# Optimization experiments

Hardware: AMD Instinct MI355X
Metric: run time of the kernel (lower is better)

The kernel has to match this reference:

```python
import jax, jax.numpy as jnp
import numpy as np

H = 128; L = 3; ODIM = 400; SCALE = 30.0

def gather_nodes(h, E_idx):
    # h: [B,N,C], E_idx: [B,N,K] -> [B,N,K,C]
    B, N, K = E_idx.shape
    C = h.shape[-1]
    idx = jnp.broadcast_to(E_idx.reshape(B, N * K, 1), (B, N * K, C))
    return jnp.take_along_axis(h, idx, axis=1).reshape(B, N, K, C)

def layer_norm(x, eps=1e-5):
    mu = jnp.mean(x, axis=-1, keepdims=True)
    var = jnp.mean((x - mu) ** 2, axis=-1, keepdims=True)
    return (x - mu) / jnp.sqrt(var + eps)

def merge_dups(h_E, inv_mapping):
    # h_E: [B,N,K,C]; inv_mapping: [B,N*K]
    B, N, K, C = h_E.shape
    flat = h_E.reshape(B, N * K, C)
    idx = jnp.broadcast_to(inv_mapping[:, :, None], (B, N * K, C))
    return jnp.take_along_axis(flat, idx, axis=1).reshape(B, N, K, C)

def setup_inputs() -> dict:
    key = jax.random.key(0)
    ks = jax.random.split(key, 40)
    B, N, K = 2, 1024, 30
    d = {}
    d['h_V0'] = jax.random.normal(ks[0], (B, N, H), jnp.float32)
    d['h_E0'] = jax.random.normal(ks[1], (B, N, K, H), jnp.float32)
    d['E_idx'] = jax.random.randint(ks[2], (B, N, K), 0, N, jnp.int32)
    d['inv_mapping'] = jax.random.randint(ks[3], (B, N * K), 0, N * K, jnp.int32)
    d['x_mask'] = jnp.ones((B, N), jnp.float32)
    s = 0.05
    d['Wv_w'] = jax.random.normal(ks[4], (H, H)) * s; d['Wv_b'] = jnp.zeros((H,))
    d['We_w'] = jax.random.normal(ks[5], (H, H)) * s; d['We_b'] = jnp.zeros((H,))
    # node MPNN layers: message MLP (3h->h->h->h) + dense FFN (h->4h->h), stacked [L,...]
    d['nW1'] = jax.random.normal(ks[6], (L, 3 * H, H)) * s; d['nb1'] = jnp.zeros((L, H))
    d['nW2'] = jax.random.normal(ks[7], (L, H, H)) * s;     d['nb2'] = jnp.zeros((L, H))
    d['nW3'] = jax.random.normal(ks[8], (L, H, H)) * s;     d['nb3'] = jnp.zeros((L, H))
    d['nWd1'] = jax.random.normal(ks[9], (L, H, 4 * H)) * s; d['nbd1'] = jnp.zeros((L, 4 * H))
    d['nWd2'] = jax.random.normal(ks[10], (L, 4 * H, H)) * s; d['nbd2'] = jnp.zeros((L, H))
    # edge MPNN layers
    d['eW1'] = jax.random.normal(ks[11], (L, 3 * H, H)) * s; d['eb1'] = jnp.zeros((L, H))
    d['eW2'] = jax.random.normal(ks[12], (L, H, H)) * s;     d['eb2'] = jnp.zeros((L, H))
    d['eW3'] = jax.random.normal(ks[13], (L, H, H)) * s;     d['eb3'] = jnp.zeros((L, H))
    d['eWd1'] = jax.random.normal(ks[14], (L, H, 4 * H)) * s; d['ebd1'] = jnp.zeros((L, 4 * H))
    d['eWd2'] = jax.random.normal(ks[15], (L, 4 * H, H)) * s; d['ebd2'] = jnp.zeros((L, H))
    d['Wout_w'] = jax.random.normal(ks[16], (H, ODIM)) * s; d['Wout_b'] = jnp.zeros((ODIM,))
    return d

def reference(h_V0, h_E0, E_idx, inv_mapping, x_mask,
              Wv_w, Wv_b, We_w, We_b,
              nW1, nb1, nW2, nb2, nW3, nb3, nWd1, nbd1, nWd2, nbd2,
              eW1, eb1, eW2, eb2, eW3, eb3, eWd1, ebd1, eWd2, ebd2,
              Wout_w, Wout_b):
    B, N, K = E_idx.shape
    h_V = h_V0 @ Wv_w + Wv_b                      # W_v embedding
    h_E = h_E0 @ We_w + We_b                      # W_e embedding
    mask_attend = gather_nodes(x_mask[..., None], E_idx)[..., 0] * x_mask[..., None]  # [B,N,K]
    for l in range(L):
        # ---- node update (NodeMPNNLayer) ----
        h_nb = gather_nodes(h_V, E_idx)                           # [B,N,K,H]
        h_i = jnp.broadcast_to(h_V[:, :, None, :], h_nb.shape)
        h_EV = jnp.concatenate([h_i, h_nb, h_E], axis=-1)         # [B,N,K,3H]
        m = jax.nn.relu(h_EV @ nW1[l] + nb1[l])
        m = jax.nn.relu(m @ nW2[l] + nb2[l])
        m = m @ nW3[l] + nb3[l]
        m = m * mask_attend[..., None]
        dh = jnp.sum(m, axis=-2) / SCALE
        h_V = layer_norm(h_V + dh)
        dh = jax.nn.relu(h_V @ nWd1[l] + nbd1[l]) @ nWd2[l] + nbd2[l]
        h_V = layer_norm(h_V + dh)
        h_V = h_V * x_mask[..., None]
        # ---- edge update (EdgeMPNNLayer) ----
        h_j = gather_nodes(h_V, E_idx)
        h_i = jnp.broadcast_to(h_V[:, :, None, :], h_j.shape)
        h_EV = jnp.concatenate([h_i, h_E, h_j], axis=-1)          # [B,N,K,3H]
        m = jax.nn.relu(h_EV @ eW1[l] + eb1[l])
        m = jax.nn.relu(m @ eW2[l] + eb2[l])
        m = m @ eW3[l] + eb3[l]
        h_E = layer_norm(h_E + m)
        dh = jax.nn.relu(h_E @ eWd1[l] + ebd1[l]) @ eWd2[l] + ebd2[l]
        h_E = layer_norm(h_E + dh)
        h_E = h_E * mask_attend[..., None]
    etab = h_E @ Wout_w + Wout_b                                  # [B,N,K,400]
    etab = merge_dups(etab, inv_mapping)
    return etab
```

## Files before the change

### kernel.cpp

```cpp
#include <hip/hip_runtime.h>
#include <hip/hip_bf16.h>
#include <stdint.h>


typedef __bf16 bf16_t;
typedef __attribute__((ext_vector_type(8))) __bf16 bf16x8;
typedef __attribute__((ext_vector_type(4))) float f32x4;

#define B_    2
#define N_    1024
#define KN    30
#define H_    128
#define L_    3
#define ODIM_ 400
#define NK    (N_ * KN)
#define RT    (B_ * N_ * KN)
#define BN_   (B_ * N_)

#define EPI_PLAIN 0
#define EPI_RELU  1
#define EPI_F32   2
#define EPI_LN    4
#define EPI_OUT   5

__device__ __forceinline__ float wred(float v) {
#pragma unroll
  for (int off = 32; off > 0; off >>= 1) v += __shfl_xor(v, off, 64);
  return v;
}

__device__ __forceinline__ void gld16(const bf16_t* g, bf16_t* l) {
  __builtin_amdgcn_global_load_lds(
      (__attribute__((address_space(1))) void*)(g),
      (__attribute__((address_space(3))) void*)(l), 16, 0, 0);
}

template<int NI>
__device__ __forceinline__ void mmN(const bf16_t* __restrict__ Ah,
                                    const bf16_t* __restrict__ Bh,
                                    int wm, int wn, int fm, int q, int fx,
                                    f32x4 (&acc)[4][NI])
{
#pragma unroll
  for (int h = 0; h < 2; ++h) {
    const int slot = ((((h << 2) | q) ^ fx) << 3);
    bf16x8 af[4], bfv[NI];
#pragma unroll
    for (int mi = 0; mi < 4; ++mi)
      af[mi] = *reinterpret_cast<const bf16x8*>(
          &Ah[(wm * 64 + mi * 16 + fm) * 64 + slot]);
#pragma unroll
    for (int ni = 0; ni < NI; ++ni)
      bfv[ni] = *reinterpret_cast<const bf16x8*>(
          &Bh[(wn * (NI * 16) + ni * 16 + fm) * 64 + slot]);
#pragma unroll
    for (int mi = 0; mi < 4; ++mi)
#pragma unroll
      for (int ni = 0; ni < NI; ++ni)
        acc[mi][ni] = __builtin_amdgcn_mfma_f32_16x16x32_bf16(
            af[mi], bfv[ni], acc[mi][ni], 0, 0, 0);
  }
}

struct GCArgs {
  const bf16_t* Ain;
  const bf16_t* W1; int koff1; int ldw1;
  const bf16_t* W2; const bf16_t* b2;
  const bf16_t* W3; const bf16_t* b3;
  const float* U; const float* G; const int* E;
  const float* ma;
  float* Agg;
  const bf16_t* Wd1; const bf16_t* bd1;
  const bf16_t* Wd2; const bf16_t* bd2;
  const float* mvec;
  bf16_t* outF;
  const bf16_t* Wug; const bf16_t* bug;
  float* Uo; float* Go;
};

template<int MODE>
__global__ __launch_bounds__(256, 2) void gc(GCArgs a)
{
  __shared__ __align__(16) bf16_t bufA[2][8192];
  __shared__ __align__(16) bf16_t bufB[2][8192];
  __shared__ __align__(16) bf16_t Ws[8192];
  float* lnS  = (float*)Ws;
  float* lnS2 = lnS + 256;
  float* aggS = (float*)Ws;

  const int tid = threadIdx.x;
  const int w = tid >> 6, l = tid & 63;
  const int wm = w & 1, wn = w >> 1;
  const int row0 = blockIdx.x * 128;
  const int lr = l >> 3;
  const int kg8 = ((l & 7) ^ lr) << 3;
  const int fm = l & 15, q = l >> 4, fx = fm & 7;

  auto stage128 = [&](const bf16_t* W, int ldw, int koff) {
    const bf16_t* gb = W + (size_t)(w * 32 + lr) * ldw + koff + kg8;
#pragma unroll
    for (int s = 0; s < 4; ++s)
      gld16(gb + (size_t)(s * 8) * ldw, &Ws[w * 2048 + s * 512]);
  };
  auto stage64 = [&](const bf16_t* W, int ldw, int koff) {
    const bf16_t* gb = W + (size_t)(w * 16 + lr) * ldw + koff + kg8;
#pragma unroll
    for (int s = 0; s < 2; ++s)
      gld16(gb + (size_t)(s * 8) * ldw, &Ws[w * 1024 + s * 512]);
  };

  auto do_gemm = [&](const bf16_t* SRC, const bf16_t* W, int koff, int ldw,
                     f32x4 (&acc)[4][4]) {
#pragma unroll
    for (int kt = 0; kt < 2; ++kt) {
      __syncthreads();
      stage128(W, ldw, koff + kt * 64);
      __syncthreads();
      mmN<4>(SRC + kt * 8192, Ws, wm, wn, fm, q, fx, acc);
    }
  };

  auto wb = [&](f32x4 (&acc)[4][4], bf16_t* dst) {
#pragma unroll
    for (int mi = 0; mi < 4; ++mi)
#pragma unroll
      for (int rr = 0; rr < 4; ++rr) {
        int row = wm * 64 + mi * 16 + q * 4 + rr;
#pragma unroll
        for (int ni = 0; ni < 4; ++ni) {
          int cl = ni * 16 + fm;
          dst[wn * 8192 + row * 64 +
              ((((cl >> 3) ^ (row & 7)) << 3) | (cl & 7))] =
              (bf16_t)acc[mi][ni][rr];
        }
      }
  };

  {
    bf16_t* dst = (MODE == 2) ? bufB[0] : bufA[0];
    const bf16_t* gb = a.Ain + (size_t)(row0 + w * 32 + lr) * 128 + kg8;
#pragma unroll
    for (int kt = 0; kt < 2; ++kt)
#pragma unroll
      for (int s = 0; s < 4; ++s)
        gld16(gb + (size_t)(s * 8) * 128 + kt * 64,
              dst + kt * 8192 + w * 2048 + s * 512);
  }

  if constexpr (MODE <= 1) {
    f32x4 acc1[4][4] = {};
    do_gemm(bufA[0], a.W1, a.koff1, a.ldw1, acc1);
#pragma unroll
    for (int mi = 0; mi < 4; ++mi)
#pragma unroll
      for (int rr = 0; rr < 4; ++rr) {
        int rg = row0 + wm * 64 + mi * 16 + q * 4 + rr;
        const float* Ur = a.U + (size_t)(rg / KN) * 128;
        const float* Gr = a.G + (size_t)((rg / NK) * N_ + a.E[rg]) * 128;
#pragma unroll
        for (int ni = 0; ni < 4; ++ni) {
          int col = wn * 64 + ni * 16 + fm;
          acc1[mi][ni][rr] = fmaxf(acc1[mi][ni][rr] + Ur[col] + Gr[col], 0.f);
        }
      }
    wb(acc1, bufB[0]);

    f32x4 acc2[4][4] = {};
    do_gemm(bufB[0], a.W2, 0, 128, acc2);
#pragma unroll
    for (int mi = 0; mi < 4; ++mi)
#pragma unroll
      for (int rr = 0; rr < 4; ++rr)
#pragma unroll
        for (int ni = 0; ni < 4; ++ni) {
          int col = wn * 64 + ni * 16 + fm;
          acc2[mi][ni][rr] = fmaxf(acc2[mi][ni][rr] + (float)a.b2[col], 0.f);
        }
    __syncthreads();
    wb(acc2, bufB[0]);

    f32x4 acc3[4][4] = {};
    do_gemm(bufB[0], a.W3, 0, 128, acc3);

    if constexpr (MODE == 0) {
      __syncthreads();
      for (int i = tid; i < 768; i += 256) aggS[i] = 0.f;
      __syncthreads();
      const int nb0 = row0 / KN;
#pragma unroll
      for (int mi = 0; mi < 4; ++mi)
#pragma unroll
        for (int rr = 0; rr < 4; ++rr) {
          int rg = row0 + wm * 64 + mi * 16 + q * 4 + rr;
          float mav = a.ma[rg];
          int nl = rg / KN - nb0;
#pragma unroll
          for (int ni = 0; ni < 4; ++ni) {
            int col = wn * 64 + ni * 16 + fm;
            atomicAdd(&aggS[nl * 128 + col],
                      (acc3[mi][ni][rr] + (float)a.b3[col]) * mav);
          }
        }
      __syncthreads();
      const int nbL = (row0 + 127) / KN;
      for (int i = tid; i < 768; i += 256) {
        int ng = nb0 + (i >> 7);
        if (ng <= nbL)
          atomicAdd(&a.Agg[(size_t)ng * 128 + (i & 127)], aggS[i]);
      }
      return;
    } else {
      __syncthreads();
#pragma unroll
      for (int mi = 0; mi < 4; ++mi)
#pragma unroll
        for (int rr = 0; rr < 4; ++rr) {
          int lrow = wm * 64 + mi * 16 + q * 4 + rr;
          float s = 0.f, s2 = 0.f;
#pragma unroll
          for (int ni = 0; ni < 4; ++ni) {
            int cl = ni * 16 + fm;
            float rv = (float)bufA[wn][lrow * 64 +
                ((((cl >> 3) ^ (lrow & 7)) << 3) | (cl & 7))];
            float v = acc3[mi][ni][rr] + (float)a.b3[wn * 64 + cl] + rv;
            acc3[mi][ni][rr] = v;
            s += v; s2 += v * v;
          }
#pragma unroll
          for (int d = 1; d < 16; d <<= 1) {
            s += __shfl_xor(s, d, 64); s2 += __shfl_xor(s2, d, 64);
          }
          if (fm == (mi * 4 + rr)) { lnS[wn * 128 + lrow] = s;
                                     lnS2[wn * 128 + lrow] = s2; }
        }
      __syncthreads();
#pragma unroll
      for (int mi = 0; mi < 4; ++mi)
#pragma unroll
        for (int rr = 0; rr < 4; ++rr) {
          int lrow = wm * 64 + mi * 16 + q * 4 + rr;
          float st = lnS[lrow] + lnS[128 + lrow];
          float st2 = lnS2[lrow] + lnS2[128 + lrow];
          float mu = st * (1.f / 128.f);
          float var = fmaxf(st2 * (1.f / 128.f) - mu * mu, 0.f);
          float rstd = rsqrtf(var + 1e-5f);
#pragma unroll
          for (int ni = 0; ni < 4; ++ni) {
            int cl = ni * 16 + fm;
            bufB[wn][lrow * 64 +
                ((((cl >> 3) ^ (lrow & 7)) << 3) | (cl & 7))] =
                (bf16_t)((acc3[mi][ni][rr] - mu) * rstd);
          }
        }
    }
  }

  {
    f32x4 accF[4][4] = {};
#pragma unroll 1
    for (int c = 0; c < 8; ++c) {
      const bf16_t* W1c = a.Wd1 + (size_t)(c * 64) * 128;
      f32x4 accH[4][2] = {};
#pragma unroll
      for (int kt = 0; kt < 2; ++kt) {
        __syncthreads();
        stage64(W1c, 128, kt * 64);
        __syncthreads();
        mmN<2>(bufB[0] + kt * 8192, Ws, wm, wn, fm, q, fx, accH);
      }
#pragma unroll
      for (int mi = 0; mi < 4; ++mi)
#pragma unroll
        for (int rr = 0; rr < 4; ++rr) {
          int row = wm * 64 + mi * 16 + q * 4 + rr;
#pragma unroll
          for (int ni = 0; ni < 2; ++ni) {
            int cH = wn * 32 + ni * 16 + fm;
            float hv = fmaxf(accH[mi][ni][rr] +
                             (float)a.bd1[c * 64 + cH], 0.f);
            bufA[0][row * 64 +
                ((((cH >> 3) ^ (row & 7)) << 3) | (cH & 7))] = (bf16_t)hv;
          }
        }
      __syncthreads();
      stage128(a.Wd2, 512, c * 64);
      __syncthreads();
      mmN<4>(bufA[0], Ws, wm, wn, fm, q, fx, accF);
    }

    __syncthreads();
#pragma unroll
    for (int mi = 0; mi < 4; ++mi)
#pragma unroll
      for (int rr = 0; rr < 4; ++rr) {
        int lrow = wm * 64 + mi * 16 + q * 4 + rr;
        float s = 0.f, s2 = 0.f;
#pragma unroll
        for (int ni = 0; ni < 4; ++ni) {
          int cl = ni * 16 + fm;
          float xv = (float)bufB[wn][lrow * 64 +
              ((((cl >> 3) ^ (lrow & 7)) << 3) | (cl & 7))];
          float v = accF[mi][ni][rr] + (float)a.bd2[wn * 64 + cl] + xv;
          accF[mi][ni][rr] = v;
          s += v; s2 += v * v;
        }
#pragma unroll
        for (int d = 1; d < 16; d <<= 1) {
          s += __shfl_xor(s, d, 64); s2 += __shfl_xor(s2, d, 64);
        }
        if (fm == (mi * 4 + rr)) { lnS[wn * 128 + lrow] = s;
                                   lnS2[wn * 128 + lrow] = s2; }
      }
    __syncthreads();
#pragma unroll
    for (int mi = 0; mi < 4; ++mi)
#pragma unroll
      for (int rr = 0; rr < 4; ++rr) {
        int lrow = wm * 64 + mi * 16 + q * 4 + rr;
        size_t rg = (size_t)(row0 + lrow);
        float st = lnS[lrow] + lnS[128 + lrow];
        float st2 = lnS2[lrow] + lnS2[128 + lrow];
        float mu = st * (1.f / 128.f);
        float var = fmaxf(st2 * (1.f / 128.f) - mu * mu, 0.f);
        float rstd = rsqrtf(var + 1e-5f);
        float mk = a.mvec[rg];
#pragma unroll
        for (int ni = 0; ni < 4; ++ni) {
          int col = wn * 64 + ni * 16 + fm;
          float ov = (accF[mi][ni][rr] - mu) * rstd * mk;
          a.outF[rg * 128 + col] = (bf16_t)ov;
          if constexpr (MODE == 2) accF[mi][ni][rr] = ov;
        }
      }

    if constexpr (MODE == 2) {
      __syncthreads();
      wb(accF, bufB[0]);
      f32x4 accU[4][4] = {};
      do_gemm(bufB[0], a.Wug, 0, 384, accU);
#pragma unroll
      for (int mi = 0; mi < 4; ++mi)
#pragma unroll
        for (int rr = 0; rr < 4; ++rr) {
          size_t rg = (size_t)(row0 + wm * 64 + mi * 16 + q * 4 + rr);
#pragma unroll
          for (int ni = 0; ni < 4; ++ni) {
            int col = wn * 64 + ni * 16 + fm;
            a.Uo[rg * 128 + col] = accU[mi][ni][rr] + (float)a.bug[col];
          }
        }
      f32x4 accG[4][4] = {};
      do_gemm(bufB[0], a.Wug, 256, 384, accG);
#pragma unroll
      for (int mi = 0; mi < 4; ++mi)
#pragma unroll
        for (int rr = 0; rr < 4; ++rr) {
          size_t rg = (size_t)(row0 + wm * 64 + mi * 16 + q * 4 + rr);
#pragma unroll
          for (int ni = 0; ni < 4; ++ni) {
            int col = wn * 64 + ni * 16 + fm;
            a.Go[rg * 128 + col] = accG[mi][ni][rr];
          }
        }
    }
  }
}

__global__ __launch_bounds__(256) void gk(
    const bf16_t* __restrict__ A, int lda,
    const bf16_t* __restrict__ Bt, int ldb, int koff,
    const bf16_t* __restrict__ bias,
    int N, int K, int epi,
    bf16_t* __restrict__ C,
    float* __restrict__ Cf, float* __restrict__ Cf1, int koff1,
    const float* __restrict__ U, const float* __restrict__ G,
    const int* __restrict__ E_idx,
    bf16_t* __restrict__ resid, const float* __restrict__ mvec, int row0g,
    const int* __restrict__ inv, const int* __restrict__ flag,
    void* __restrict__ outp)
{
  __shared__ __align__(16) bf16_t As[128 * 64];
  __shared__ __align__(16) bf16_t Bs[128 * 64];
  __shared__ float lnS[2][128];
  __shared__ float lnS2[2][128];

  float* CfD = Cf;
  if (epi == EPI_F32 && blockIdx.z == 1) { koff = koff1; bias = nullptr; CfD = Cf1; }

  const int tid = threadIdx.x;
  const int w = tid >> 6, l = tid & 63;
  const int wm = w & 1, wn = w >> 1;
  const int row0 = blockIdx.y * 128;
  const int col0 = blockIdx.x * 128;
  const int lr = l >> 3;
  const int kg8 = ((l & 7) ^ lr) << 3;

  const bf16_t* ap[4];
  const bf16_t* bp[4];
#pragma unroll
  for (int s = 0; s < 4; ++s) {
    int rA = row0 + w * 32 + s * 8 + lr;
    const bf16_t* abase;
    if (epi == EPI_OUT) {
      int bb = rA / NK;
      abase = A + (size_t)(bb * NK + inv[rA]) * lda;
    } else {
      abase = A + (size_t)rA * lda;
    }
    ap[s] = abase + kg8;
    int rB = col0 + w * 32 + s * 8 + lr;
    if (rB >= N) rB = N - 1;
    bp[s] = Bt + (size_t)rB * ldb + koff + kg8;
  }

  const int fm = l & 15, q = l >> 4, fx = fm & 7;
  f32x4 acc[4][4] = {};

  for (int kt = 0; kt < K; kt += 64) {
    __syncthreads();
#pragma unroll
    for (int s = 0; s < 4; ++s)
      gld16(ap[s] + kt, &As[w * 2048 + s * 512]);
#pragma unroll
    for (int s = 0; s < 4; ++s)
      gld16(bp[s] + kt, &Bs[w * 2048 + s * 512]);
    __syncthreads();
#pragma unroll
    for (int h = 0; h < 2; ++h) {
      bf16x8 af[4], bfv[4];
#pragma unroll
      for (int mi = 0; mi < 4; ++mi)
        af[mi] = *reinterpret_cast<const bf16x8*>(
            &As[(wm * 64 + mi * 16 + fm) * 64 + ((((h << 2) | q) ^ fx) << 3)]);
#pragma unroll
      for (int ni = 0; ni < 4; ++ni)
        bfv[ni] = *reinterpret_cast<const bf16x8*>(
            &Bs[(wn * 64 + ni * 16 + fm) * 64 + ((((h << 2) | q) ^ fx) << 3)]);
#pragma unroll
      for (int mi = 0; mi < 4; ++mi)
#pragma unroll
        for (int ni = 0; ni < 4; ++ni)
          acc[mi][ni] = __builtin_amdgcn_mfma_f32_16x16x32_bf16(
              af[mi], bfv[ni], acc[mi][ni], 0, 0, 0);
    }
  }

  if (epi <= EPI_F32) {
#pragma unroll
    for (int ni = 0; ni < 4; ++ni) {
      int col = col0 + wn * 64 + ni * 16 + fm;
      if (col >= N) continue;
      float bv = bias ? (float)bias[col] : 0.f;
#pragma unroll
      for (int mi = 0; mi < 4; ++mi)
#pragma unroll
        for (int rr = 0; rr < 4; ++rr) {
          size_t rg = (size_t)(row0g + row0 + wm * 64 + mi * 16 + q * 4 + rr);
          float v = acc[mi][ni][rr] + bv;
          if (epi == EPI_RELU) v = fmaxf(v, 0.f);
          if (epi == EPI_F32) CfD[rg * N + col] = v;
          else                C[rg * N + col] = (bf16_t)v;
        }
    }
  } else if (epi == EPI_LN) {
#pragma unroll
    for (int mi = 0; mi < 4; ++mi)
#pragma unroll
      for (int rr = 0; rr < 4; ++rr) {
        int lrow = wm * 64 + mi * 16 + q * 4 + rr;
        size_t rg = (size_t)(row0g + row0 + lrow);
        float s = 0.f, s2 = 0.f;
#pragma unroll
        for (int ni = 0; ni < 4; ++ni) {
          int col = wn * 64 + ni * 16 + fm;
          float v = acc[mi][ni][rr] + (bias ? (float)bias[col] : 0.f)
                    + (float)resid[rg * 128 + col];
          acc[mi][ni][rr] = v;
          s += v; s2 += v * v;
        }
#pragma unroll
        for (int d = 1; d < 16; d <<= 1) {
          s += __shfl_xor(s, d, 64); s2 += __shfl_xor(s2, d, 64);
        }
        if (fm == (mi * 4 + rr)) { lnS[wn][lrow] = s; lnS2[wn][lrow] = s2; }
      }
    __syncthreads();
#pragma unroll
    for (int mi = 0; mi < 4; ++mi)
#pragma unroll
      for (int rr = 0; rr < 4; ++rr) {
        int lrow = wm * 64 + mi * 16 + q * 4 + rr;
        size_t rg = (size_t)(row0g + row0 + lrow);
        float st = lnS[0][lrow] + lnS[1][lrow];
        float st2 = lnS2[0][lrow] + lnS2[1][lrow];
        float mu = st * (1.f / 128.f);
        float var = fmaxf(st2 * (1.f / 128.f) - mu * mu, 0.f);
        float rstd = rsqrtf(var + 1e-5f);
        float mk = mvec ? mvec[rg] : 1.f;
#pragma unroll
        for (int ni = 0; ni < 4; ++ni) {
          int col = wn * 64 + ni * 16 + fm;
          resid[rg * 128 + col] = (bf16_t)((acc[mi][ni][rr] - mu) * rstd * mk);
        }
      }
  } else if (epi == EPI_OUT) {
    const int fl = *flag;
#pragma unroll
    for (int ni = 0; ni < 4; ++ni) {
      int col = col0 + wn * 64 + ni * 16 + fm;
      if (col >= ODIM_) continue;
      float bv = bias ? (float)bias[col] : 0.f;
#pragma unroll
      for (int mi = 0; mi < 4; ++mi)
#pragma unroll
        for (int rr = 0; rr < 4; ++rr) {
          size_t rg = (size_t)(row0 + wm * 64 + mi * 16 + q * 4 + rr);
          float v = acc[mi][ni][rr] + bv;
          size_t idx = rg * ODIM_ + col;
          if (fl) ((bf16_t*)outp)[idx] = (bf16_t)v;
          else    ((float*)outp)[idx]  = v;
        }
    }
  }
}

__global__ void flag_kernel(const uint32_t* __restrict__ xm_raw,
                            int* __restrict__ flag)
{
  if (threadIdx.x == 0 && blockIdx.x == 0)
    *flag = (xm_raw[0] == 0x3F803F80u) ? 1 : 0;
}

struct ConvSeg { const void* src; void* dst; int n; int K; int N; };
struct ConvArgs { ConvSeg s[29]; };

__global__ __launch_bounds__(256) void conv_kernel(
    ConvArgs a, int nseg, int total8, const int* __restrict__ flag)
{
  int t = blockIdx.x * 256 + threadIdx.x;
  if (t >= total8) return;
  const int fl = *flag;
  int seg = 0, t8 = t;
  while (seg < nseg - 1 && t8 >= (a.s[seg].n >> 3)) { t8 -= a.s[seg].n >> 3; ++seg; }
  const ConvSeg sg = a.s[seg];
  const int e = t8 << 3;
  float vals[8];
  if (fl) {
    union { uint4 v; bf16_t b[8]; } u;
    u.v = *((const uint4*)sg.src + t8);
#pragma unroll
    for (int j = 0; j < 8; ++j) vals[j] = (float)u.b[j];
  } else {
    const float* sp = (const float*)sg.src + e;
#pragma unroll
    for (int j = 0; j < 8; ++j) vals[j] = sp[j];
  }
  if (sg.N == 0) {
    union { uint4 v; bf16_t b[8]; } o;
#pragma unroll
    for (int j = 0; j < 8; ++j) o.b[j] = (bf16_t)vals[j];
    *((uint4*)sg.dst + t8) = o.v;
  } else {
    const int KN_ = sg.K * sg.N;
    const int lay = e / KN_;
    const int rem = e - lay * KN_;
    const int k = rem / sg.N;
    const int n0 = rem - k * sg.N;
    bf16_t* dp = (bf16_t*)sg.dst + (size_t)lay * KN_ + k;
#pragma unroll
    for (int j = 0; j < 8; ++j)
      dp[(size_t)(n0 + j) * sg.K] = (bf16_t)vals[j];
  }
}

__global__ __launch_bounds__(256) void mask_kernel(
    const bf16_t* __restrict__ xm, const int* __restrict__ E_idx,
    float* __restrict__ ma, float* __restrict__ xmf)
{
  int r = blockIdx.x * 256 + threadIdx.x;
  if (r >= RT) return;
  if (r < BN_) xmf[r] = (float)xm[r];
  int b = r / NK;
  int n = (r / KN) % N_;
  ma[r] = (float)xm[b * N_ + E_idx[r]] * (float)xm[b * N_ + n];
}

__global__ __launch_bounds__(256) void zero_kernel(float* __restrict__ p, int n)
{
  int i = blockIdx.x * 256 + threadIdx.x;
  if (i < n) p[i] = 0.f;
}

__global__ __launch_bounds__(128) void node_ln_kernel(
    float* __restrict__ Agg, bf16_t* __restrict__ hV)
{
  int bn = blockIdx.x;
  int c = threadIdx.x;
  size_t idx = (size_t)bn * H_ + c;
  float v = (float)hV[idx] + Agg[idx] * (1.0f / 30.0f);
  Agg[idx] = 0.f;
  __shared__ float red[4];
  float ss = wred(v), s2 = wred(v * v);
  int w = c >> 6, lane = c & 63;
  if (lane == 0) { red[w * 2] = ss; red[w * 2 + 1] = s2; }
  __syncthreads();
  float tot = red[0] + red[2], tot2 = red[1] + red[3];
  float mu = tot * (1.f / 128.f);
  float var = fmaxf(tot2 * (1.f / 128.f) - mu * mu, 0.f);
  float rstd = rsqrtf(var + 1e-5f);
  hV[idx] = (bf16_t)((v - mu) * rstd);
}

extern "C" void kernel_launch(void* const* d_in, const int* in_sizes, int n_in,
                              void* d_out, int out_size, void* d_ws, size_t ws_size,
                              hipStream_t stream)
{
  const int* E_idx  = (const int*)d_in[2];
  const int* invmap = (const int*)d_in[3];

  char* ws = (char*)d_ws;
  size_t woff = 0;
  auto walloc = [&](size_t bytes) -> char* {
    char* p = ws + woff; woff += (bytes + 255) & ~(size_t)255; return p;
  };
  int*    flag  = (int*)walloc(4);
  bf16_t* WtOut = (bf16_t*)walloc((size_t)51200 * 2);
  bf16_t* outbc = (bf16_t*)walloc((size_t)400 * 2);
  bf16_t* hE    = (bf16_t*)walloc((size_t)RT * H_ * 2);

  char* ob = (char*)d_out;
  bf16_t* t0 = (bf16_t*)ob;
  bf16_t* t1 = (bf16_t*)(ob + (size_t)RT * H_ * 2);
  size_t ooff = (size_t)RT * H_ * 2 * 2;
  auto oalloc = [&](size_t bytes) -> char* {
    char* p = ob + ooff; ooff += (bytes + 255) & ~(size_t)255; return p;
  };
  bf16_t* WtV  = (bf16_t*)oalloc(16384 * 2);
  bf16_t* bvc  = (bf16_t*)oalloc(128 * 2);
  bf16_t* WtE  = (bf16_t*)oalloc(16384 * 2);
  bf16_t* bec  = (bf16_t*)oalloc(128 * 2);
  bf16_t* Wtn1 = (bf16_t*)oalloc((size_t)147456 * 2);
  bf16_t* nb1c = (bf16_t*)oalloc(384 * 2);
  bf16_t* Wtn2 = (bf16_t*)oalloc((size_t)49152 * 2);
  bf16_t* nb2c = (bf16_t*)oalloc(384 * 2);
  bf16_t* Wtn3 = (bf16_t*)oalloc((size_t)49152 * 2);
  bf16_t* nb3c = (bf16_t*)oalloc(384 * 2);
  bf16_t* Wtnd1 = (bf16_t*)oalloc((size_t)196608 * 2);
  bf16_t* nbd1c = (bf16_t*)oalloc(1536 * 2);
  bf16_t* Wtnd2 = (bf16_t*)oalloc((size_t)196608 * 2);
  bf16_t* nbd2c = (bf16_t*)oalloc(384 * 2);
  bf16_t* Wte1 = (bf16_t*)oalloc((size_t)147456 * 2);
  bf16_t* eb1c = (bf16_t*)oalloc(384 * 2);
  bf16_t* Wte2 = (bf16_t*)oalloc((size_t)49152 * 2);
  bf16_t* eb2c = (bf16_t*)oalloc(384 * 2);
  bf16_t* Wte3 = (bf16_t*)oalloc((size_t)49152 * 2);
  bf16_t* eb3c = (bf16_t*)oalloc(384 * 2);
  bf16_t* Wted1 = (bf16_t*)oalloc((size_t)196608 * 2);
  bf16_t* ebd1c = (bf16_t*)oalloc(1536 * 2);
  bf16_t* Wted2 = (bf16_t*)oalloc((size_t)196608 * 2);
  bf16_t* ebd2c = (bf16_t*)oalloc(384 * 2);
  float*  Ubuf = (float*)oalloc((size_t)BN_ * 128 * 4);
  float*  Gbuf = (float*)oalloc((size_t)BN_ * 128 * 4);
  bf16_t* hV   = (bf16_t*)oalloc((size_t)BN_ * 128 * 2);
  float*  ma   = (float*)oalloc((size_t)RT * 4);
  bf16_t* xm   = (bf16_t*)oalloc((size_t)BN_ * 2);
  float*  xmf  = (float*)oalloc((size_t)BN_ * 4);
  float*  Abuf = (float*)oalloc((size_t)BN_ * 128 * 4);

  ConvArgs ca;
  struct D { int idx; void* dst; int K; int N; };
  const D dl[29] = {
    {0, t1, 0, 0}, {1, t0, 0, 0}, {4, xm, 0, 0},
    {5, WtV, 128, 128}, {6, bvc, 0, 0}, {7, WtE, 128, 128}, {8, bec, 0, 0},
    {9, Wtn1, 384, 128}, {10, nb1c, 0, 0}, {11, Wtn2, 128, 128}, {12, nb2c, 0, 0},
    {13, Wtn3, 128, 128}, {14, nb3c, 0, 0},
    {15, Wtnd1, 128, 512}, {16, nbd1c, 0, 0}, {17, Wtnd2, 512, 128}, {18, nbd2c, 0, 0},
    {19, Wte1, 384, 128}, {20, eb1c, 0, 0}, {21, Wte2, 128, 128}, {22, eb2c, 0, 0},
    {23, Wte3, 128, 128}, {24, eb3c, 0, 0},
    {25, Wted1, 128, 512}, {26, ebd1c, 0, 0}, {27, Wted2, 512, 128}, {28, ebd2c, 0, 0},
    {29, WtOut, 128, 400}, {30, outbc, 0, 0}
  };
  int total8 = 0;
  for (int i = 0; i < 29; ++i) {
    ca.s[i].src = d_in[dl[i].idx];
    ca.s[i].dst = dl[i].dst;
    ca.s[i].n   = in_sizes[dl[i].idx];
    ca.s[i].K   = dl[i].K;
    ca.s[i].N   = dl[i].N;
    total8 += ca.s[i].n >> 3;
  }

  auto g = [&](dim3 grid, const bf16_t* A, int lda, const bf16_t* Bt, int ldb,
               int koff, const bf16_t* bias, int N, int K, int epi,
               bf16_t* C, float* Cf, float* Cf1, int koff1,
               bf16_t* resid, const float* mvec, int row0g) {
    gk<<<grid, 256, 0, stream>>>(A, lda, Bt, ldb, koff, bias, N, K, epi,
        C, Cf, Cf1, koff1, Ubuf, Gbuf, E_idx, resid, mvec, row0g,
        invmap, flag, d_out);
  };
  const float* NOM = nullptr;

  flag_kernel<<<1, 64, 0, stream>>>((const uint32_t*)d_in[4], flag);
  conv_kernel<<<(total8 + 255) / 256, 256, 0, stream>>>(ca, 29, total8, flag);
  mask_kernel<<<RT / 256, 256, 0, stream>>>(xm, E_idx, ma, xmf);
  zero_kernel<<<(BN_ * 128) / 256, 256, 0, stream>>>(Abuf, BN_ * 128);

  g(dim3(1, BN_ / 128), t1, 128, WtV, 128, 0, bvc, 128, 128, EPI_PLAIN,
    hV, nullptr, nullptr, 0, nullptr, NOM, 0);
  g(dim3(1, RT / 128), t0, 128, WtE, 128, 0, bec, 128, 128, EPI_PLAIN,
    hE, nullptr, nullptr, 0, nullptr, NOM, 0);

  for (int l = 0; l < L_; ++l) {
    g(dim3(1, BN_ / 128, 2), hV, 128, Wtn1 + (size_t)l * 49152, 384, 0,
      nb1c + l * 128, 128, 128, EPI_F32,
      nullptr, Ubuf, Gbuf, 128, nullptr, NOM, 0);
    {
      GCArgs na{};
      na.Ain = hE;
      na.W1 = Wtn1 + (size_t)l * 49152; na.koff1 = 256; na.ldw1 = 384;
      na.W2 = Wtn2 + (size_t)l * 16384; na.b2 = nb2c + l * 128;
      na.W3 = Wtn3 + (size_t)l * 16384; na.b3 = nb3c + l * 128;
      na.U = Ubuf; na.G = Gbuf; na.E = E_idx;
      na.ma = ma; na.Agg = Abuf;
      gc<0><<<RT / 128, 256, 0, stream>>>(na);
    }
    node_ln_kernel<<<BN_, 128, 0, stream>>>(Abuf, hV);
    {
      GCArgs nf{};
      nf.Ain = hV;
      nf.Wd1 = Wtnd1 + (size_t)l * 65536; nf.bd1 = nbd1c + l * 512;
      nf.Wd2 = Wtnd2 + (size_t)l * 65536; nf.bd2 = nbd2c + l * 128;
      nf.mvec = xmf; nf.outF = hV;
      nf.Wug = Wte1 + (size_t)l * 49152; nf.bug = eb1c + l * 128;
      nf.Uo = Ubuf; nf.Go = Gbuf;
      gc<2><<<BN_ / 128, 256, 0, stream>>>(nf);
    }
    {
      GCArgs ea{};
      ea.Ain = hE;
      ea.W1 = Wte1 + (size_t)l * 49152; ea.koff1 = 128; ea.ldw1 = 384;
      ea.W2 = Wte2 + (size_t)l * 16384; ea.b2 = eb2c + l * 128;
      ea.W3 = Wte3 + (size_t)l * 16384; ea.b3 = eb3c + l * 128;
      ea.U = Ubuf; ea.G = Gbuf; ea.E = E_idx;
      ea.Wd1 = Wted1 + (size_t)l * 65536; ea.bd1 = ebd1c + l * 512;
      ea.Wd2 = Wted2 + (size_t)l * 65536; ea.bd2 = ebd2c + l * 128;
      ea.mvec = ma; ea.outF = hE;
      gc<1><<<RT / 128, 256, 0, stream>>>(ea);
    }
  }

  g(dim3(4, RT / 128), hE, 128, WtOut, 128, 0, outbc, ODIM_, 128, EPI_OUT,
    nullptr, nullptr, nullptr, 0, nullptr, NOM, 0);
}
```

Before: 723.5 us.

## Software-pipeline FFN weight staging with async LDS loads and explicit waitcnt barriers

The dense FFN loop now prefetches the next Wd1 chunk and the current Wd2 chunk into separate LDS regions (Ws and bufA[1]) with async global-to-LDS loads. Explicit vmcnt waits plus raw barriers replace the paired __syncthreads, so loads overlap with the MFMA work. It also raises wave priority around the matrix multiplies and reuses one accumulator array across the GEMM stages to cut register pressure. The risk is subtle LDS hazards if the vmcnt counts or buffer aliasing are wrong.

New measurement: 701.1 us. 1.03x faster.

```diff
diff --git a/kernel.cpp b/kernel.cpp
--- a/kernel.cpp
+++ b/kernel.cpp
@@ -33,6 +33,22 @@
   __builtin_amdgcn_global_load_lds(
       (__attribute__((address_space(1))) void*)(g),
       (__attribute__((address_space(3))) void*)(l), 16, 0, 0);
+}
+
+__device__ __forceinline__ void barL() {
+  asm volatile("s_waitcnt lgkmcnt(0)" ::: "memory");
+  __builtin_amdgcn_s_barrier();
+  __builtin_amdgcn_sched_barrier(0);
+}
+__device__ __forceinline__ void wait_v4_bar() {
+  asm volatile("s_waitcnt vmcnt(4) lgkmcnt(0)" ::: "memory");
+  __builtin_amdgcn_s_barrier();
+  __builtin_amdgcn_sched_barrier(0);
+}
+__device__ __forceinline__ void wait_v0_bar() {
+  asm volatile("s_waitcnt vmcnt(0) lgkmcnt(0)" ::: "memory");
+  __builtin_amdgcn_s_barrier();
+  __builtin_amdgcn_sched_barrier(0);
 }
 
 template<int NI>
@@ -102,11 +118,19 @@
     for (int s = 0; s < 4; ++s)
       gld16(gb + (size_t)(s * 8) * ldw, &Ws[w * 2048 + s * 512]);
   };
-  auto stage64 = [&](const bf16_t* W, int ldw, int koff) {
-    const bf16_t* gb = W + (size_t)(w * 16 + lr) * ldw + koff + kg8;
-#pragma unroll
-    for (int s = 0; s < 2; ++s)
-      gld16(gb + (size_t)(s * 8) * ldw, &Ws[w * 1024 + s * 512]);
+  auto stageWd1 = [&](int c) {
+    const bf16_t* gb = a.Wd1 + (size_t)(c * 64 + w * 16 + lr) * 128 + kg8;
+#pragma unroll
+    for (int s = 0; s < 2; ++s) {
+      gld16(gb + (size_t)(s * 8) * 128,      &Ws[w * 1024 + s * 512]);
+      gld16(gb + (size_t)(s * 8) * 128 + 64, &Ws[4096 + w * 1024 + s * 512]);
+    }
+  };
+  auto stageWd2 = [&](int c) {
+    const bf16_t* gb = a.Wd2 + (size_t)(w * 32 + lr) * 512 + c * 64 + kg8;
+#pragma unroll
+    for (int s = 0; s < 4; ++s)
+      gld16(gb + (size_t)(s * 8) * 512, &bufA[1][w * 2048 + s * 512]);
   };
 
   auto do_gemm = [&](const bf16_t* SRC, const bf16_t* W, int koff, int ldw,
@@ -136,6 +160,15 @@
       }
   };
 
+  f32x4 accA[4][4];
+  auto zeroA = [&]() {
+#pragma unroll
+    for (int mi = 0; mi < 4; ++mi)
+#pragma unroll
+      for (int ni = 0; ni < 4; ++ni)
+        accA[mi][ni] = f32x4{0.f, 0.f, 0.f, 0.f};
+  };
+
   {
     bf16_t* dst = (MODE == 2) ? bufB[0] : bufA[0];
     const bf16_t* gb = a.Ain + (size_t)(row0 + w * 32 + lr) * 128 + kg8;
@@ -146,10 +179,11 @@
         gld16(gb + (size_t)(s * 8) * 128 + kt * 64,
               dst + kt * 8192 + w * 2048 + s * 512);
   }
+  if constexpr (MODE == 2) stageWd1(0);
 
   if constexpr (MODE <= 1) {
-    f32x4 acc1[4][4] = {};
-    do_gemm(bufA[0], a.W1, a.koff1, a.ldw1, acc1);
+    zeroA();
+    do_gemm(bufA[0], a.W1, a.koff1, a.ldw1, accA);
 #pragma unroll
     for (int mi = 0; mi < 4; ++mi)
 #pragma unroll
@@ -160,13 +194,13 @@
 #pragma unroll
         for (int ni = 0; ni < 4; ++ni) {
           int col = wn * 64 + ni * 16 + fm;
-          acc1[mi][ni][rr] = fmaxf(acc1[mi][ni][rr] + Ur[col] + Gr[col], 0.f);
+          accA[mi][ni][rr] = fmaxf(accA[mi][ni][rr] + Ur[col] + Gr[col], 0.f);
         }
       }
-    wb(acc1, bufB[0]);
-
-    f32x4 acc2[4][4] = {};
-    do_gemm(bufB[0], a.W2, 0, 128, acc2);
+    wb(accA, bufB[0]);
+
+    zeroA();
+    do_gemm(bufB[0], a.W2, 0, 128, accA);
 #pragma unroll
     for (int mi = 0; mi < 4; ++mi)
 #pragma unroll
@@ -174,13 +208,13 @@
 #pragma unroll
         for (int ni = 0; ni < 4; ++ni) {
           int col = wn * 64 + ni * 16 + fm;
-          acc2[mi][ni][rr] = fmaxf(acc2[mi][ni][rr] + (float)a.b2[col], 0.f);
+          accA[mi][ni][rr] = fmaxf(accA[mi][ni][rr] + (float)a.b2[col], 0.f);
         }
     __syncthreads();
-    wb(acc2, bufB[0]);
-
-    f32x4 acc3[4][4] = {};
-    do_gemm(bufB[0], a.W3, 0, 128, acc3);
+    wb(accA, bufB[0]);
+
+    zeroA();
+    do_gemm(bufB[0], a.W3, 0, 128, accA);
 
     if constexpr (MODE == 0) {
       __syncthreads();
@@ -198,7 +232,7 @@
           for (int ni = 0; ni < 4; ++ni) {
             int col = wn * 64 + ni * 16 + fm;
             atomicAdd(&aggS[nl * 128 + col],
-                      (acc3[mi][ni][rr] + (float)a.b3[col]) * mav);
+                      (accA[mi][ni][rr] + (float)a.b3[col]) * mav);
           }
         }
       __syncthreads();
@@ -222,8 +256,8 @@
             int cl = ni * 16 + fm;
             float rv = (float)bufA[wn][lrow * 64 +
                 ((((cl >> 3) ^ (lrow & 7)) << 3) | (cl & 7))];
-            float v = acc3[mi][ni][rr] + (float)a.b3[wn * 64 + cl] + rv;
-            acc3[mi][ni][rr] = v;
+            float v = accA[mi][ni][rr] + (float)a.b3[wn * 64 + cl] + rv;
+            accA[mi][ni][rr] = v;
             s += v; s2 += v * v;
           }
 #pragma unroll
@@ -233,7 +267,7 @@
           if (fm == (mi * 4 + rr)) { lnS[wn * 128 + lrow] = s;
                                      lnS2[wn * 128 + lrow] = s2; }
         }
-      __syncthreads();
+      barL();
 #pragma unroll
       for (int mi = 0; mi < 4; ++mi)
 #pragma unroll
@@ -249,25 +283,25 @@
             int cl = ni * 16 + fm;
             bufB[wn][lrow * 64 +
                 ((((cl >> 3) ^ (lrow & 7)) << 3) | (cl & 7))] =
-                (bf16_t)((acc3[mi][ni][rr] - mu) * rstd);
+                (bf16_t)((accA[mi][ni][rr] - mu) * rstd);
           }
         }
+      barL();
+      stageWd1(0);
     }
   }
 
   {
-    f32x4 accF[4][4] = {};
+    zeroA();
 #pragma unroll 1
     for (int c = 0; c < 8; ++c) {
-      const bf16_t* W1c = a.Wd1 + (size_t)(c * 64) * 128;
+      stageWd2(c);
+      wait_v4_bar();
       f32x4 accH[4][2] = {};
-#pragma unroll
-      for (int kt = 0; kt < 2; ++kt) {
-        __syncthreads();
-        stage64(W1c, 128, kt * 64);
-        __syncthreads();
-        mmN<2>(bufB[0] + kt * 8192, Ws, wm, wn, fm, q, fx, accH);
-      }
+      __builtin_amdgcn_s_setprio(1);
+      mmN<2>(bufB[0],        Ws,        wm, wn, fm, q, fx, accH);
+      mmN<2>(bufB[0] + 8192, Ws + 4096, wm, wn, fm, q, fx, accH);
+      __builtin_amdgcn_s_setprio(0);
 #pragma unroll
       for (int mi = 0; mi < 4; ++mi)
 #pragma unroll
@@ -282,10 +316,21 @@
                 ((((cH >> 3) ^ (row & 7)) << 3) | (cH & 7))] = (bf16_t)hv;
           }
         }
-      __syncthreads();
-      stage128(a.Wd2, 512, c * 64);
-      __syncthreads();
-      mmN<4>(bufA[0], Ws, wm, wn, fm, q, fx, accF);
+      barL();
+      if (c < 7) {
+        stageWd1(c + 1);
+        asm volatile("s_waitcnt vmcnt(4) lgkmcnt(0)" ::: "memory");
+      } else {
+        asm volatile("s_waitcnt vmcnt(0) lgkmcnt(0)" ::: "memory");
+      }
+      __builtin_amdgcn_s_barrier();
+      __builtin_amdgcn_sched_barrier(0);
+      __builtin_amdgcn_s_setprio(1);
+      mmN<4>(bufA[0], bufA[1], wm, wn, fm, q, fx, accA);
+      __builtin_amdgcn_s_setprio(0);
+      __builtin_amdgcn_sched_barrier(0);
+      __builtin_amdgcn_s_barrier();
+      __builtin_amdgcn_sched_barrier(0);
     }
 
     __syncthreads();
@@ -300,8 +345,8 @@
           int cl = ni * 16 + fm;
           float xv = (float)bufB[wn][lrow * 64 +
               ((((cl >> 3) ^ (lrow & 7)) << 3) | (cl & 7))];
-          float v = accF[mi][ni][rr] + (float)a.bd2[wn * 64 + cl] + xv;
-          accF[mi][ni][rr] = v;
+          float v = accA[mi][ni][rr] + (float)a.bd2[wn * 64 + cl] + xv;
+          accA[mi][ni][rr] = v;
           s += v; s2 += v * v;
         }
 #pragma unroll
@@ -327,17 +372,17 @@
 #pragma unroll
         for (int ni = 0; ni < 4; ++ni) {
           int col = wn * 64 + ni * 16 + fm;
-          float ov = (accF[mi][ni][rr] - mu) * rstd * mk;
+          float ov = (accA[mi][ni][rr] - mu) * rstd * mk;
           a.outF[rg * 128 + col] = (bf16_t)ov;
-          if constexpr (MODE == 2) accF[mi][ni][rr] = ov;
+          if constexpr (MODE == 2) accA[mi][ni][rr] = ov;
         }
       }
 
     if constexpr (MODE == 2) {
       __syncthreads();
-      wb(accF, bufB[0]);
-      f32x4 accU[4][4] = {};
-      do_gemm(bufB[0], a.Wug, 0, 384, accU);
+      wb(accA, bufB[0]);
+      zeroA();
+      do_gemm(bufB[0], a.Wug, 0, 384, accA);
 #pragma unroll
       for (int mi = 0; mi < 4; ++mi)
 #pragma unroll
@@ -346,11 +391,11 @@
 #pragma unroll
           for (int ni = 0; ni < 4; ++ni) {
             int col = wn * 64 + ni * 16 + fm;
-            a.Uo[rg * 128 + col] = accU[mi][ni][rr] + (float)a.bug[col];
+            a.Uo[rg * 128 + col] = accA[mi][ni][rr] + (float)a.bug[col];
           }
         }
-      f32x4 accG[4][4] = {};
-      do_gemm(bufB[0], a.Wug, 256, 384, accG);
+      zeroA();
+      do_gemm(bufB[0], a.Wug, 256, 384, accA);
 #pragma unroll
       for (int mi = 0; mi < 4; ++mi)
 #pragma unroll
@@ -359,7 +404,7 @@
 #pragma unroll
           for (int ni = 0; ni < 4; ++ni) {
             int col = wn * 64 + ni * 16 + fm;
-            a.Go[rg * 128 + col] = accG[mi][ni][rr];
+            a.Go[rg * 128 + col] = accA[mi][ni][rr];
           }
         }
     }
```
